# Optimization experiments

Hardware: AMD Instinct MI355X
Metric: run time of the kernel (lower is better)

The kernel has to match this reference:

```python
import jax, jax.numpy as jnp
import numpy as np

T, B, DIM = 1024, 32, 1024
H, N = 8, 64
INIT_BETA_BIAS = 2.0
EPS = 1e-6


def setup_inputs() -> dict:
    key = jax.random.key(0)
    ks = jax.random.split(key, 5)
    scale = 1.0 / np.sqrt(DIM)  # xavier-ish
    return {
        "x": jax.random.normal(ks[0], (T, B, DIM), dtype=jnp.float32),
        "W_k": jax.random.normal(ks[1], (H * N, DIM), dtype=jnp.float32) * scale,
        "W_v": jax.random.normal(ks[2], (H * N, DIM), dtype=jnp.float32) * scale,
        "W_q": jax.random.normal(ks[3], (H * N, DIM), dtype=jnp.float32) * scale,
        "W_beta": jax.random.normal(ks[4], (H * N, DIM), dtype=jnp.float32) * scale,
        "b_beta": jnp.full((H, N), INIT_BETA_BIAS, dtype=jnp.float32),
    }


def reference(x, W_k, W_v, W_q, W_beta, b_beta):
    Tn, Bn, D = x.shape
    Hn, n = b_beta.shape
    xf = x.reshape(Tn * Bn, D)
    k_all = (xf @ W_k.T).reshape(Tn, Bn, Hn, n)
    v_all = (xf @ W_v.T).reshape(Tn, Bn, Hn, n)
    q_all = (xf @ W_q.T).reshape(Tn, Bn, Hn, n)
    beta_all = jax.nn.sigmoid((xf @ W_beta.T).reshape(Tn, Bn, Hn, n) + b_beta)
    k_norm = k_all / (jnp.linalg.norm(k_all, axis=-1, keepdims=True) + EPS)

    def step(S, inp):
        k, v, q, beta = inp  # each [B, H, n]
        retrieved = jnp.einsum('bhij,bhj->bhi', S, k)
        delta = v - retrieved
        outer = jnp.einsum('bhi,bhj->bhij', delta, k)
        S = jnp.tanh(beta[..., None] * S + outer)
        Sq = jnp.einsum('bhij,bhj->bhi', S, q)
        out = Sq * jax.nn.silu(Sq)  # [B, H, n]
        return S, out.reshape(Bn, Hn * n)

    S0 = jnp.zeros((Bn, Hn, n, n), dtype=x.dtype)
    S_final, output = jax.lax.scan(step, S0, (k_norm, v_all, q_all, beta_all))
    return output, S_final  # output: [T, B, H*n]
```

## Files before the change

kernel.cpp:

```cpp
#include <hip/hip_runtime.h>
#include <stdint.h>

#define TSTEPS 1024
#define BATCH  32
#define DIMK   1024
#define HEADS  8
#define NHEAD  64
#define NPROJ  2048
#define MROWS  (TSTEPS*BATCH)

typedef _Float16 f16;
typedef _Float16 f16x2 __attribute__((ext_vector_type(2)));
typedef _Float16 f16x4 __attribute__((ext_vector_type(4)));
typedef _Float16 f16x8 __attribute__((ext_vector_type(8)));
typedef float    f32x2 __attribute__((ext_vector_type(2)));
typedef float    f32x4 __attribute__((ext_vector_type(4)));
typedef unsigned int u32;

#define AS_GLOBAL __attribute__((address_space(1)))
#define AS_LDS    __attribute__((address_space(3)))

#define C2LOG2E 2.8853900817779268f

__device__ __forceinline__ void load_lds_16B(const void* g, void* l){
  __builtin_amdgcn_global_load_lds((const AS_GLOBAL u32*)g, (AS_LDS u32*)l, 16, 0, 0);
}

__device__ __forceinline__ float sigmoid_fast(float x){
  return __builtin_amdgcn_rcpf(1.0f + __expf(-x));
}

__device__ __forceinline__ float exp2_fast(float x){
#if __has_builtin(__builtin_amdgcn_exp2f)
  return __builtin_amdgcn_exp2f(x);
#else
  return __expf(0.6931471805599453f * x);
#endif
}

__device__ __forceinline__ float fdot2(f16x2 a, f16x2 b, float c){
#if __has_builtin(__builtin_amdgcn_fdot2)
  typedef __fp16 h16x2 __attribute__((ext_vector_type(2)));
  return __builtin_amdgcn_fdot2(__builtin_bit_cast(h16x2, a),
                                __builtin_bit_cast(h16x2, b), c, false);
#else
  return fmaf((float)a[1], (float)b[1], fmaf((float)a[0], (float)b[0], c));
#endif
}

__device__ __forceinline__ f16x2 pack2(float a, float b){
#if __has_builtin(__builtin_amdgcn_cvt_pkrtz)
  return __builtin_bit_cast(f16x2, __builtin_amdgcn_cvt_pkrtz(a, b));
#else
  f16x2 r = { (f16)a, (f16)b };
  return r;
#endif
}

template<int CTRL>
__device__ __forceinline__ float dpp_add(float r){
  int x = __builtin_amdgcn_update_dpp(__builtin_bit_cast(int, r),
                                      __builtin_bit_cast(int, r),
                                      CTRL, 0xf, 0xf, false);
  return r + __builtin_bit_cast(float, x);
}
__device__ __forceinline__ float dpp_reduce16(float r){
  r = dpp_add<0x121>(r);
  r = dpp_add<0x122>(r);
  r = dpp_add<0x124>(r);
  r = dpp_add<0x128>(r);
  return r;
}

__global__ __launch_bounds__(256) void cast_kernel(const float4* __restrict__ src,
                                                   f16x4* __restrict__ dst, int n4){
  int i = blockIdx.x*blockDim.x + threadIdx.x;
  int stride = gridDim.x*blockDim.x;
  for (; i < n4; i += stride){
    float4 v = src[i];
    f16x4 o = { (f16)v.x, (f16)v.y, (f16)v.z, (f16)v.w };
    dst[i] = o;
  }
}

#define BM 128
#define BN 128
#define BK 32

__global__ __launch_bounds__(256) void gemm_xwT(const f16* __restrict__ A,
                                                const f16* __restrict__ B,
                                                f16* __restrict__ Zo){
  __shared__ f16 sA[BM*BK];
  __shared__ f16 sB[BN*BK];
  const int t = threadIdx.x;
  const int w = t >> 6;
  const int l = t & 63;
  const int bm = blockIdx.x;
  const int bn = blockIdx.y;
  const int wr = w >> 1, wc = w & 1;

  f32x4 acc[4][4] = {};

  const int srow = t >> 2;
  const int scol = (t & 3) * 8;
  const f16* gA0 = A + (size_t)(bm*BM + srow)*DIMK + scol;
  const f16* gB0 = B + (size_t)(bn*BN + srow)*DIMK + scol;
  char* sAb = (char*)sA;
  char* sBb = (char*)sB;
  const int ldsw = w*1024;

  for (int kk = 0; kk < DIMK/BK; ++kk){
    const f16* pa = gA0 + kk*BK;
    const f16* pb = gB0 + kk*BK;
    load_lds_16B(pa,           sAb + ldsw);
    load_lds_16B(pa + 64*DIMK, sAb + ldsw + 4096);
    load_lds_16B(pb,           sBb + ldsw);
    load_lds_16B(pb + 64*DIMK, sBb + ldsw + 4096);
    __syncthreads();

    f16x8 af[4], bf[4];
    #pragma unroll
    for (int mi=0; mi<4; ++mi){
      int arow = wr*64 + mi*16 + (l & 15);
      af[mi] = *(const f16x8*)(sAb + arow*64 + (l>>4)*16);
    }
    #pragma unroll
    for (int ni=0; ni<4; ++ni){
      int brow = wc*64 + ni*16 + (l & 15);
      bf[ni] = *(const f16x8*)(sBb + brow*64 + (l>>4)*16);
    }
    #pragma unroll
    for (int mi=0; mi<4; ++mi)
      #pragma unroll
      for (int ni=0; ni<4; ++ni)
        acc[mi][ni] = __builtin_amdgcn_mfma_f32_16x16x32_f16(af[mi], bf[ni], acc[mi][ni], 0, 0, 0);
    __syncthreads();
  }

  const int crow0 = bm*BM + wr*64 + (l>>4)*4;
  const int ccol0 = bn*BN + wc*64 + (l & 15);
  #pragma unroll
  for (int ni=0; ni<4; ++ni){
    int n = ccol0 + ni*16;
    int stream = n >> 9;
    int hh = (n >> 6) & 7;
    int e = n & 63;
    int eidx = (stream==0) ? e : (stream==2) ? 64+e : (stream==1) ? 128+2*e : 129+2*e;
    #pragma unroll
    for (int mi=0; mi<4; ++mi)
      #pragma unroll
      for (int r=0; r<4; ++r){
        int m = crow0 + mi*16 + r;
        int ti = m >> 5, bi = m & 31;
        size_t zi = ((size_t)(bi*8 + hh)*1024 + ti)*256 + eidx;
        Zo[zi] = (f16)acc[mi][ni][r];
      }
  }
}

__global__ __launch_bounds__(256) void prep_kernel(f16* __restrict__ Z,
                                                   const float* __restrict__ b_beta){
  int wid = blockIdx.x*4 + (threadIdx.x >> 6);
  int l = threadIdx.x & 63;
  int h = (wid >> 10) & 7;
  f16* z = Z + (size_t)wid * 256;
  float k  = (float)z[l];
  float br = (float)z[129 + 2*l];
  float ss = k*k;
  #pragma unroll
  for (int d=1; d<64; d<<=1) ss += __shfl_xor(ss, d);
  z[l]       = (f16)(k * __builtin_amdgcn_rcpf(__builtin_sqrtf(ss) + 1e-6f));
  z[129+2*l] = (f16)(C2LOG2E * sigmoid_fast(br + b_beta[h*NHEAD + l]));
}

#define STAGE_STEPS 64
#define STAGE_F16   (STAGE_STEPS*256)

__global__ __launch_bounds__(1024) void scan_kernel(const f16* __restrict__ Z,
                                                    float* __restrict__ out,
                                                    float* __restrict__ S_out){
  const int p = blockIdx.x;
  const int b = p >> 3, h = p & 7;
  const int t = threadIdx.x;
  const int w = t >> 6;
  const int lane = t & 63;
  const int row = t >> 4;
  const int g   = t & 15;

  __shared__ f16 lds[2*STAGE_F16];

  f32x2 S01 = {0.f,0.f}, S23 = {0.f,0.f};
  f16x2 P0 = {}, P1 = {};

  const char* Zp = (const char*)(Z + (size_t)p * (TSTEPS*256));
  float* outp = out + (size_t)b*512 + h*NHEAD + row;
  char* ldsb = (char*)lds;

  {
    const char* src = Zp + w*2048 + lane*16;
    load_lds_16B(src,        ldsb + w*2048);
    load_lds_16B(src + 1024, ldsb + w*2048 + 1024);
  }
  __syncthreads();

  #pragma unroll 1
  for (int st=0; st<TSTEPS/STAGE_STEPS; ++st){
    if (st < TSTEPS/STAGE_STEPS - 1){
      const char* src = Zp + (st+1)*(STAGE_F16*2) + w*2048 + lane*16;
      char* dst = ldsb + ((st+1)&1)*(STAGE_F16*2) + w*2048;
      load_lds_16B(src,        dst);
      load_lds_16B(src + 1024, dst + 1024);
    }

    const f16* buf = lds + (st&1)*STAGE_F16;
    #pragma unroll 4
    for (int s=0; s<STAGE_STEPS; ++s){
      const f16* ps = buf + s*256;
      f16x4 k4 = *(const f16x4*)(ps + g*4);
      f16x4 q4 = *(const f16x4*)(ps + 64 + g*4);
      f16x2 vb = *(const f16x2*)(ps + 128 + row*2);

      uint2 ku = __builtin_bit_cast(uint2, k4);
      uint2 qu = __builtin_bit_cast(uint2, q4);
      f16x2 kl = __builtin_bit_cast(f16x2, ku.x), kh = __builtin_bit_cast(f16x2, ku.y);
      f16x2 ql = __builtin_bit_cast(f16x2, qu.x), qh = __builtin_bit_cast(f16x2, qu.y);
      float v  = (float)vb[0];
      float bb = (float)vb[1];

      float r = fdot2(P1, kh, fdot2(P0, kl, 0.f));
      r = dpp_reduce16(r);
      float dl = (v - r) * C2LOG2E;

      f32x2 d2  = { dl, dl };
      f32x2 bb2 = { bb, bb };
      f32x2 k01 = { (float)kl[0], (float)kl[1] };
      f32x2 k23 = { (float)kh[0], (float)kh[1] };
      f32x2 arg01 = bb2*S01 + d2*k01;
      f32x2 arg23 = bb2*S23 + d2*k23;

      f32x2 e01 = { exp2_fast(arg01.x), exp2_fast(arg01.y) };
      f32x2 e23 = { exp2_fast(arg23.x), exp2_fast(arg23.y) };
      f32x2 one2 = { 1.f, 1.f };
      e01 += one2;  e23 += one2;
      f32x2 t01 = { __builtin_amdgcn_rcpf(e01.x), __builtin_amdgcn_rcpf(e01.y) };
      f32x2 t23 = { __builtin_amdgcn_rcpf(e23.x), __builtin_amdgcn_rcpf(e23.y) };
      f32x2 m2 = { -2.f, -2.f };
      S01 = m2*t01 + one2;
      S23 = m2*t23 + one2;
      P0 = pack2(S01.x, S01.y);
      P1 = pack2(S23.x, S23.y);

      float sq = fdot2(P1, qh, fdot2(P0, ql, 0.f));
      sq = dpp_reduce16(sq);
      if (g == 0) outp[(size_t)(st*STAGE_STEPS + s) * (BATCH*512)] = sq;
    }
    __syncthreads();
  }

  size_t sbase = ((size_t)p*NHEAD + row)*NHEAD + g*4;
  float4 v4 = { S01.x, S01.y, S23.x, S23.y };
  *(float4*)(S_out + sbase) = v4;
}

__global__ __launch_bounds__(256) void silu_kernel(float4* __restrict__ o, int n4){
  int i = blockIdx.x*blockDim.x + threadIdx.x;
  int stride = gridDim.x*blockDim.x;
  for (; i < n4; i += stride){
    float4 v = o[i];
    v.x = v.x*v.x*sigmoid_fast(v.x);
    v.y = v.y*v.y*sigmoid_fast(v.y);
    v.z = v.z*v.z*sigmoid_fast(v.z);
    v.w = v.w*v.w*sigmoid_fast(v.w);
    o[i] = v;
  }
}

extern "C" void kernel_launch(void* const* d_in, const int* in_sizes, int n_in,
                              void* d_out, int out_size, void* d_ws, size_t ws_size,
                              hipStream_t stream){
  const float* x  = (const float*)d_in[0];
  const float* Wk = (const float*)d_in[1];
  const float* Wv = (const float*)d_in[2];
  const float* Wq = (const float*)d_in[3];
  const float* Wb = (const float*)d_in[4];
  const float* bb = (const float*)d_in[5];

  float* out = (float*)d_out;
  float* Sf  = out + (size_t)TSTEPS*BATCH*512;

  char* ws = (char*)d_ws;
  f16* Zh = (f16*)ws;
  f16* xh = (f16*)(ws + 134217728);
  f16* wh = (f16*)(ws + 134217728 + 67108864);

  cast_kernel<<<2048, 256, 0, stream>>>((const float4*)x,  (f16x4*)xh, (MROWS*DIMK)/4);
  cast_kernel<<<512,  256, 0, stream>>>((const float4*)Wk, (f16x4*)(wh + 0*524288), 524288/4);
  cast_kernel<<<512,  256, 0, stream>>>((const float4*)Wv, (f16x4*)(wh + 1*524288), 524288/4);
  cast_kernel<<<512,  256, 0, stream>>>((const float4*)Wq, (f16x4*)(wh + 2*524288), 524288/4);
  cast_kernel<<<512,  256, 0, stream>>>((const float4*)Wb, (f16x4*)(wh + 3*524288), 524288/4);

  dim3 g(MROWS/BM, NPROJ/BN);
  gemm_xwT<<<g, 256, 0, stream>>>(xh, wh, Zh);

  prep_kernel<<<(TSTEPS*BATCH*HEADS)/4, 256, 0, stream>>>(Zh, bb);

  scan_kernel<<<256, 1024, 0, stream>>>(Zh, out, Sf);

  silu_kernel<<<2048, 256, 0, stream>>>((float4*)out, (TSTEPS*BATCH*512)/4);
}
```

Baseline: 840.9 us.

## Store GEMM output row-major and gather per-head streams in scan loader

The GEMM epilogue now writes the projection output as a plain row-major [T*B, 2048] matrix instead of scattering it into a per-(batch,head) timestep-major interleaved layout. The prep kernel and the scan kernel's async LDS loader are rewritten to index this layout, with each thread gathering 16-byte chunks of k, v, q and beta for its head. This is meant to make the GEMM stores contiguous rather than scattered 2-byte writes. The cost is that the scan's global loads become strided 16B gathers across rows, and the scan reads v and beta separately rather than as one interleaved pair.

```diff
diff --git a/kernel.cpp b/kernel.cpp
--- a/kernel.cpp
+++ b/kernel.cpp
@@ -89,7 +89,7 @@
 
 __global__ __launch_bounds__(256) void gemm_xwT(const f16* __restrict__ A,
                                                 const f16* __restrict__ B,
-                                                f16* __restrict__ Zo){
+                                                f16* __restrict__ C){
   __shared__ f16 sA[BM*BK];
   __shared__ f16 sB[BN*BK];
   const int t = threadIdx.x;
@@ -140,50 +140,41 @@
   const int crow0 = bm*BM + wr*64 + (l>>4)*4;
   const int ccol0 = bn*BN + wc*64 + (l & 15);
   #pragma unroll
-  for (int ni=0; ni<4; ++ni){
-    int n = ccol0 + ni*16;
-    int stream = n >> 9;
-    int hh = (n >> 6) & 7;
-    int e = n & 63;
-    int eidx = (stream==0) ? e : (stream==2) ? 64+e : (stream==1) ? 128+2*e : 129+2*e;
+  for (int mi=0; mi<4; ++mi)
     #pragma unroll
-    for (int mi=0; mi<4; ++mi)
+    for (int ni=0; ni<4; ++ni)
       #pragma unroll
-      for (int r=0; r<4; ++r){
-        int m = crow0 + mi*16 + r;
-        int ti = m >> 5, bi = m & 31;
-        size_t zi = ((size_t)(bi*8 + hh)*1024 + ti)*256 + eidx;
-        Zo[zi] = (f16)acc[mi][ni][r];
-      }
-  }
-}
-
-__global__ __launch_bounds__(256) void prep_kernel(f16* __restrict__ Z,
+      for (int r=0; r<4; ++r)
+        C[(size_t)(crow0 + mi*16 + r)*NPROJ + ccol0 + ni*16] = (f16)acc[mi][ni][r];
+}
+
+__global__ __launch_bounds__(256) void prep_kernel(f16* __restrict__ Y,
                                                    const float* __restrict__ b_beta){
-  int wid = blockIdx.x*4 + (threadIdx.x >> 6);
+  int g = blockIdx.x*4 + (threadIdx.x >> 6);
   int l = threadIdx.x & 63;
-  int h = (wid >> 10) & 7;
-  f16* z = Z + (size_t)wid * 256;
-  float k  = (float)z[l];
-  float br = (float)z[129 + 2*l];
+  int h = g & 7;
+  f16* y = Y + (size_t)(g >> 3)*NPROJ + h*NHEAD + l;
+  float k  = (float)y[0];
+  float br = (float)y[1536];
   float ss = k*k;
   #pragma unroll
   for (int d=1; d<64; d<<=1) ss += __shfl_xor(ss, d);
-  z[l]       = (f16)(k * __builtin_amdgcn_rcpf(__builtin_sqrtf(ss) + 1e-6f));
-  z[129+2*l] = (f16)(C2LOG2E * sigmoid_fast(br + b_beta[h*NHEAD + l]));
+  y[0]    = (f16)(k * __builtin_amdgcn_rcpf(__builtin_sqrtf(ss) + 1e-6f));
+  y[1536] = (f16)(C2LOG2E * sigmoid_fast(br + b_beta[h*NHEAD + l]));
 }
 
 #define STAGE_STEPS 64
 #define STAGE_F16   (STAGE_STEPS*256)
-
-__global__ __launch_bounds__(1024) void scan_kernel(const f16* __restrict__ Z,
+#define STAGE_BYTES 32768
+#define NSTAGES     (TSTEPS/STAGE_STEPS)
+
+__global__ __launch_bounds__(1024) void scan_kernel(const f16* __restrict__ Y,
                                                     float* __restrict__ out,
                                                     float* __restrict__ S_out){
   const int p = blockIdx.x;
   const int b = p >> 3, h = p & 7;
   const int t = threadIdx.x;
   const int w = t >> 6;
-  const int lane = t & 63;
   const int row = t >> 4;
   const int g   = t & 15;
 
@@ -192,40 +183,49 @@
   f32x2 S01 = {0.f,0.f}, S23 = {0.f,0.f};
   f16x2 P0 = {}, P1 = {};
 
-  const char* Zp = (const char*)(Z + (size_t)p * (TSTEPS*256));
   float* outp = out + (size_t)b*512 + h*NHEAD + row;
   char* ldsb = (char*)lds;
 
-  {
-    const char* src = Zp + w*2048 + lane*16;
-    load_lds_16B(src,        ldsb + w*2048);
-    load_lds_16B(src + 1024, ldsb + w*2048 + 1024);
-  }
+  auto mksrc = [&](int c) -> const char* {
+    int tl = c >> 5, rr = c & 31, stream = rr >> 3, e8 = rr & 7;
+    return (const char*)(Y + ((size_t)tl*BATCH + b)*NPROJ + stream*512 + h*NHEAD + e8*8);
+  };
+  const char* src0 = mksrc(t);
+  const char* src1 = mksrc(t + 1024);
+  const size_t SADV = (size_t)STAGE_STEPS*BATCH*NPROJ*sizeof(f16);
+
+  char* d0 = ldsb + w*1024;
+  char* d1 = ldsb + 16384 + w*1024;
+
+  load_lds_16B(src0, d0);
+  load_lds_16B(src1, d1);
+  src0 += SADV; src1 += SADV;
   __syncthreads();
 
   #pragma unroll 1
-  for (int st=0; st<TSTEPS/STAGE_STEPS; ++st){
-    if (st < TSTEPS/STAGE_STEPS - 1){
-      const char* src = Zp + (st+1)*(STAGE_F16*2) + w*2048 + lane*16;
-      char* dst = ldsb + ((st+1)&1)*(STAGE_F16*2) + w*2048;
-      load_lds_16B(src,        dst);
-      load_lds_16B(src + 1024, dst + 1024);
+  for (int st=0; st<NSTAGES; ++st){
+    if (st < NSTAGES-1){
+      char* dst = ldsb + ((st+1)&1)*STAGE_BYTES;
+      load_lds_16B(src0, dst + w*1024);
+      load_lds_16B(src1, dst + 16384 + w*1024);
+      src0 += SADV; src1 += SADV;
     }
 
-    const f16* buf = lds + (st&1)*STAGE_F16;
+    const char* buf = ldsb + (st&1)*STAGE_BYTES;
     #pragma unroll 4
     for (int s=0; s<STAGE_STEPS; ++s){
-      const f16* ps = buf + s*256;
-      f16x4 k4 = *(const f16x4*)(ps + g*4);
-      f16x4 q4 = *(const f16x4*)(ps + 64 + g*4);
-      f16x2 vb = *(const f16x2*)(ps + 128 + row*2);
+      const char* psb = buf + s*512;
+      f16x4 k4 = *(const f16x4*)(psb + g*8);
+      f16x4 q4 = *(const f16x4*)(psb + 256 + g*8);
+      f16 vh   = *(const f16*)(psb + 128 + row*2);
+      f16 bh   = *(const f16*)(psb + 384 + row*2);
 
       uint2 ku = __builtin_bit_cast(uint2, k4);
       uint2 qu = __builtin_bit_cast(uint2, q4);
       f16x2 kl = __builtin_bit_cast(f16x2, ku.x), kh = __builtin_bit_cast(f16x2, ku.y);
       f16x2 ql = __builtin_bit_cast(f16x2, qu.x), qh = __builtin_bit_cast(f16x2, qu.y);
-      float v  = (float)vb[0];
-      float bb = (float)vb[1];
+      float v  = (float)vh;
+      float bb = (float)bh;
 
       float r = fdot2(P1, kh, fdot2(P0, kl, 0.f));
       r = dpp_reduce16(r);
@@ -289,7 +289,7 @@
   float* Sf  = out + (size_t)TSTEPS*BATCH*512;
 
   char* ws = (char*)d_ws;
-  f16* Zh = (f16*)ws;
+  f16* Yh = (f16*)ws;
   f16* xh = (f16*)(ws + 134217728);
   f16* wh = (f16*)(ws + 134217728 + 67108864);
 
@@ -300,11 +300,11 @@
   cast_kernel<<<512,  256, 0, stream>>>((const float4*)Wb, (f16x4*)(wh + 3*524288), 524288/4);
 
   dim3 g(MROWS/BM, NPROJ/BN);
-  gemm_xwT<<<g, 256, 0, stream>>>(xh, wh, Zh);
-
-  prep_kernel<<<(TSTEPS*BATCH*HEADS)/4, 256, 0, stream>>>(Zh, bb);
-
-  scan_kernel<<<256, 1024, 0, stream>>>(Zh, out, Sf);
+  gemm_xwT<<<g, 256, 0, stream>>>(xh, wh, Yh);
+
+  prep_kernel<<<(TSTEPS*BATCH*HEADS)/4, 256, 0, stream>>>(Yh, bb);
+
+  scan_kernel<<<256, 1024, 0, stream>>>(Yh, out, Sf);
 
   silu_kernel<<<2048, 256, 0, stream>>>((float4*)out, (TSTEPS*BATCH*512)/4);
 }
```

New measurement: 763.7 us. 1.1x faster.
